# Kernel optimization log

Measured on AMD Instinct MI355X. Metric: run time of the kernel, lower is better.

## Reference

```python
import jax, jax.numpy as jnp
from jax import lax
import numpy as np

V, D_EMB, H, P, B, T = 32000, 512, 1024, 512, 32, 512
NUM_LAYERS = 2


def setup_inputs() -> dict:
    key = jax.random.key(0)
    ks = jax.random.split(key, 2 + NUM_LAYERS * 5)
    tokens = jax.random.randint(ks[0], (B, T), 0, V, dtype=jnp.int32)
    embed = jax.random.normal(ks[1], (V, D_EMB), dtype=jnp.float32) * 0.02
    inp = {"tokens": tokens, "embed": embed}
    in_dims = [D_EMB] + [P] * (NUM_LAYERS - 1)
    for l in range(NUM_LAYERS):
        kk = ks[2 + 5 * l: 7 + 5 * l]
        inp[f"Wx{l}"] = jax.random.normal(kk[0], (in_dims[l], 4 * H), dtype=jnp.float32) * 0.02
        inp[f"Wh{l}"] = jax.random.normal(kk[1], (H, 4 * H), dtype=jnp.float32) * 0.02
        inp[f"b{l}"] = jnp.zeros((4 * H,), dtype=jnp.float32)
        inp[f"Wfc{l}"] = jax.random.normal(kk[3], (H, P), dtype=jnp.float32) * 0.02
        inp[f"bfc{l}"] = jnp.zeros((P,), dtype=jnp.float32)
    return inp


def _lstm(x, Wx, Wh, b):
    # x: [B, T, D] -> [B, T, H]. Keras gate order: i, f, g(cell), o.
    Bsz = x.shape[0]
    h0 = jnp.zeros((Bsz, H), dtype=x.dtype)
    c0 = jnp.zeros((Bsz, H), dtype=x.dtype)

    # Precompute input projection for all timesteps (one big GEMM).
    xz = jnp.einsum('btd,dg->btg', x, Wx) + b  # [B, T, 4H]

    def step(carry, zt):
        h, c = carry
        z = zt + h @ Wh
        i, f, g, o = jnp.split(z, 4, axis=-1)
        c = jax.nn.sigmoid(f) * c + jax.nn.sigmoid(i) * jnp.tanh(g)
        h = jax.nn.sigmoid(o) * jnp.tanh(c)
        return (h, c), h

    _, ys = lax.scan(step, (h0, c0), jnp.swapaxes(xz, 0, 1))  # ys: [T, B, H]
    return jnp.swapaxes(ys, 0, 1)


def reference(tokens, embed, Wx0, Wh0, b0, Wfc0, bfc0, Wx1, Wh1, b1, Wfc1, bfc1):
    # inference path: dropout is identity (training=False), use_softmax=False
    x = embed[tokens]  # [B, T, D_EMB]
    layers = [(Wx0, Wh0, b0, Wfc0, bfc0), (Wx1, Wh1, b1, Wfc1, bfc1)]
    for Wx, Wh, b, Wfc, bfc in layers:
        x = _lstm(x, Wx, Wh, b)
        x = x @ Wfc + bfc  # per-layer dense projection [B, T, P]
    return x
```

## Files before the change

kernel.cpp:

```cpp
#include <hip/hip_runtime.h>
#include <cstdio>
#include <cstdint>

typedef unsigned short u16;
typedef unsigned int u32;
typedef float f32x4 __attribute__((ext_vector_type(4)));
typedef short s16x8 __attribute__((ext_vector_type(8)));

#define DI __device__ __forceinline__

#define BATCH 32
#define SEQT 512
#define HDIM 1024
#define PDIM 512
#define DEMB 512
#define G4H 4096
#define NWGR 256

DI u16 f2bf(float f) {
  u32 u = __float_as_uint(f);
  return (u16)((u + 0x7fffu + ((u >> 16) & 1u)) >> 16);
}
DI float bf2f(u16 h) { return __uint_as_float(((u32)h) << 16); }
DI void split2(float f, u16 &hi, u16 &lo) {
  hi = f2bf(f);
  lo = f2bf(f - bf2f(hi));
}
DI f32x4 mfma16(s16x8 a, s16x8 b, f32x4 c) {
  return __builtin_amdgcn_mfma_f32_16x16x32_bf16(a, b, c, 0, 0, 0);
}
DI void dma16(const void *g, void *l) {
  __builtin_amdgcn_global_load_lds((const __attribute__((address_space(1))) void *)g,
                                   (__attribute__((address_space(3))) void *)l, 16, 0, 0);
}
DI s16x8 ld128_dev(const u16 *p) {
  s16x8 r;
  asm volatile("global_load_dwordx4 %0, %1, off sc1" : "=v"(r) : "v"(p));
  return r;
}
DI void st16_dev(u16 *p, u16 v) {
  asm volatile("global_store_short %0, %1, off sc1" ::"v"(p), "v"((u32)v) : "memory");
}
DI void st32_dev(int *p, int v) {
  asm volatile("global_store_dword %0, %1, off sc1" ::"v"(p), "v"(v) : "memory");
}

__global__ void k_gather_pack(const int *__restrict__ tokens, const float *__restrict__ embed,
                              u16 *__restrict__ xhi, u16 *__restrict__ xlo) {
  int idx = blockIdx.x * 256 + threadIdx.x;
  int m = idx >> 6;
  int k8 = (idx & 63) << 3;
  int tok = tokens[m];
  const float *src = embed + (size_t)tok * DEMB + k8;
  float4 a = *(const float4 *)src;
  float4 b = *(const float4 *)(src + 4);
  float v[8] = {a.x, a.y, a.z, a.w, b.x, b.y, b.z, b.w};
  union UV { u16 h[8]; int4 v; };
  UV uh, ul;
#pragma unroll
  for (int j = 0; j < 8; ++j) split2(v[j], uh.h[j], ul.h[j]);
  size_t o = (size_t)m * DEMB + k8;
  *(int4 *)(xhi + o) = uh.v;
  *(int4 *)(xlo + o) = ul.v;
}

__global__ void k_packT(const float *__restrict__ W, u16 *__restrict__ Thi, u16 *__restrict__ Tlo,
                        int K, int N) {
  __shared__ float tile[32][33];
  int n0 = blockIdx.x * 32, k0 = blockIdx.y * 32;
  int tx = threadIdx.x, ty = threadIdx.y;
#pragma unroll
  for (int i = 0; i < 4; ++i) tile[ty + 8 * i][tx] = W[(size_t)(k0 + ty + 8 * i) * N + n0 + tx];
  __syncthreads();
#pragma unroll
  for (int i = 0; i < 4; ++i) {
    int n = ty + 8 * i;
    u16 hi, lo;
    split2(tile[tx][n], hi, lo);
    size_t o = (size_t)(n0 + n) * K + k0 + tx;
    Thi[o] = hi;
    Tlo[o] = lo;
  }
}

template <int OM>
__global__ __launch_bounds__(256, 2) void k_gemm(const u16 *__restrict__ Ahi, const u16 *__restrict__ Alo,
                                                 const u16 *__restrict__ Bhi, const u16 *__restrict__ Blo,
                                                 const float *__restrict__ bias, void *__restrict__ out0,
                                                 void *__restrict__ out1, int M, int N, int K) {
  __shared__ u16 sP[4][128 * 64];
  const int tid = threadIdx.x;
  const int w = tid >> 6, lane = tid & 63;
  const int la15 = lane & 15, la4 = lane >> 4;
  const int nbn = N >> 7;
  const int bm = blockIdx.x / nbn, bn = blockIdx.x % nbn;
  const u16 *src = (w == 0) ? Ahi : (w == 1) ? Alo : (w == 2) ? Bhi : Blo;
  const int rowbase = (w < 2) ? bm * 128 : bn * 128;
  char *lds = (char *)&sP[w][0];

  f32x4 acc[2][8] = {};
  for (int kb = 0; kb < K; kb += 64) {
#pragma unroll
    for (int i = 0; i < 16; ++i) {
      int s = i * 64 + lane;
      int row = s >> 3;
      int k16 = (s & 7) ^ (row & 7);
      dma16(src + (size_t)(rowbase + row) * K + kb + k16 * 8, lds + i * 1024);
    }
    asm volatile("s_waitcnt vmcnt(0)" ::: "memory");
    __syncthreads();
#pragma unroll
    for (int ksl = 0; ksl < 2; ++ksl) {
      s16x8 ah[2], al[2];
#pragma unroll
      for (int rf = 0; rf < 2; ++rf) {
        int row = 32 * w + 16 * rf + la15;
        int slot = row * 8 + ((4 * ksl + la4) ^ (row & 7));
        ah[rf] = *(const s16x8 *)((const char *)&sP[0][0] + slot * 16);
        al[rf] = *(const s16x8 *)((const char *)&sP[1][0] + slot * 16);
      }
#pragma unroll
      for (int cf = 0; cf < 8; ++cf) {
        int col = 16 * cf + la15;
        int slot = col * 8 + ((4 * ksl + la4) ^ (col & 7));
        s16x8 bh = *(const s16x8 *)((const char *)&sP[2][0] + slot * 16);
        s16x8 bl = *(const s16x8 *)((const char *)&sP[3][0] + slot * 16);
#pragma unroll
        for (int rf = 0; rf < 2; ++rf) {
          acc[rf][cf] = mfma16(ah[rf], bh, acc[rf][cf]);
          acc[rf][cf] = mfma16(ah[rf], bl, acc[rf][cf]);
          acc[rf][cf] = mfma16(al[rf], bh, acc[rf][cf]);
        }
      }
    }
    __syncthreads();
  }
#pragma unroll
  for (int rf = 0; rf < 2; ++rf) {
#pragma unroll
    for (int cf = 0; cf < 8; ++cf) {
      int c = bn * 128 + 16 * cf + la15;
      float bv = bias ? bias[c] : 0.f;
#pragma unroll
      for (int q = 0; q < 4; ++q) {
        int r = bm * 128 + 32 * w + 16 * rf + 4 * la4 + q;
        float v = acc[rf][cf][q] + bv;
        if (OM == 0) {
          ((u16 *)out0)[(size_t)r * N + c] = f2bf(v);
        } else if (OM == 1) {
          u16 hi, lo;
          split2(v, hi, lo);
          ((u16 *)out0)[(size_t)r * N + c] = hi;
          ((u16 *)out1)[(size_t)r * N + c] = lo;
        } else {
          int b2 = r & 31, tt = r >> 5;
          ((float *)out0)[((size_t)b2 * SEQT + tt) * PDIM + c] = v;
        }
      }
    }
  }
}

__global__ __launch_bounds__(256, 1) void k_recur(const u16 *__restrict__ xz, const float *__restrict__ Wh,
                                                  u16 *hhi, u16 *hlo, int *done, int rowmode) {
  __shared__ u16 sW[2][32 * 1024];
  __shared__ float zacc[4][16][33];
  __shared__ float sC[128];
  const int tid = threadIdx.x;
  const int w = tid >> 6, lane = tid & 63;
  const int la15 = lane & 15, la4 = lane >> 4;
  const int wg = blockIdx.x;
  const int rg = wg & 1;
  const int g = wg >> 1;

  for (int idx = tid; idx < 32 * 1024; idx += 256) {
    int zc = idx & 31;
    int k = idx >> 5;
    int gate = zc >> 3, cl = zc & 7;
    int gcol = gate * HDIM + 8 * g + cl;
    u16 hi, lo;
    split2(Wh[(size_t)k * G4H + gcol], hi, lo);
    int boff = zc * 2048 + ((((k >> 3) ^ (zc & 7))) << 4) + (k & 7) * 2;
    *(u16 *)((char *)&sW[0][0] + boff) = hi;
    *(u16 *)((char *)&sW[1][0] + boff) = lo;
  }
  if (tid < 128) sC[tid] = 0.f;
  __syncthreads();

  const int r_g = tid >> 3, hc = tid & 7;
  const int bg = 16 * rg + r_g;
  const int ks0 = 8 * w;
  const int bA = 16 * rg + la15;

  for (int t = 0; t < SEQT; ++t) {
    float xzv[4] = {0.f, 0.f, 0.f, 0.f};
    if (tid < 128) {
      size_t m = (rowmode == 0) ? ((size_t)bg * SEQT + t) : ((size_t)t * 32 + bg);
      const u16 *px = xz + m * G4H + 8 * g + hc;
#pragma unroll
      for (int gi = 0; gi < 4; ++gi) xzv[gi] = bf2f(px[(size_t)gi * HDIM]);
    }
    if (t > 0 && w == 0) {
      const int *dp = done + (size_t)(t - 1) * 256 + rg * 128 + lane;
      for (long tries = 0;; ++tries) {
        int a = __hip_atomic_load(dp, __ATOMIC_RELAXED, __HIP_MEMORY_SCOPE_AGENT);
        int b = __hip_atomic_load(dp + 64, __ATOMIC_RELAXED, __HIP_MEMORY_SCOPE_AGENT);
        if (__all((a & b) == 1)) break;
        if (tries > (1L << 22)) break;
        __builtin_amdgcn_s_sleep(1);
      }
    }
    __syncthreads();
    if (t > 0) {
      const u16 *ph = hhi + ((size_t)(t - 1) * 32 + bA) * HDIM;
      const u16 *pl = hlo + ((size_t)(t - 1) * 32 + bA) * HDIM;
      s16x8 ahi[8], alo[8];
#pragma unroll
      for (int j8 = 0; j8 < 8; ++j8) {
        int k = 32 * (ks0 + j8) + 8 * la4;
        ahi[j8] = ld128_dev(ph + k);
        alo[j8] = ld128_dev(pl + k);
      }
      asm volatile("s_waitcnt vmcnt(0)" ::: "memory");
      __builtin_amdgcn_sched_barrier(0);
      f32x4 acc[2] = {};
#pragma unroll
      for (int j8 = 0; j8 < 8; ++j8) {
#pragma unroll
        for (int cf = 0; cf < 2; ++cf) {
          int zc = 16 * cf + la15;
          int slot = (4 * (ks0 + j8) + la4) ^ (zc & 7);
          int boff = zc * 2048 + (slot << 4);
          s16x8 bh = *(const s16x8 *)((const char *)&sW[0][0] + boff);
          s16x8 bl = *(const s16x8 *)((const char *)&sW[1][0] + boff);
          acc[cf] = mfma16(ahi[j8], bh, acc[cf]);
          acc[cf] = mfma16(ahi[j8], bl, acc[cf]);
          acc[cf] = mfma16(alo[j8], bh, acc[cf]);
        }
      }
#pragma unroll
      for (int cf = 0; cf < 2; ++cf)
#pragma unroll
        for (int q = 0; q < 4; ++q) zacc[w][4 * la4 + q][16 * cf + la15] = acc[cf][q];
    }
    __syncthreads();
    if (tid < 128) {
      float z4[4];
#pragma unroll
      for (int gi = 0; gi < 4; ++gi) {
        float s = xzv[gi];
        if (t > 0) {
          int zc = gi * 8 + hc;
          s += zacc[0][r_g][zc] + zacc[1][r_g][zc] + zacc[2][r_g][zc] + zacc[3][r_g][zc];
        }
        z4[gi] = s;
      }
      float ig = 1.f / (1.f + expf(-z4[0]));
      float fg = 1.f / (1.f + expf(-z4[1]));
      float gg = tanhf(z4[2]);
      float og = 1.f / (1.f + expf(-z4[3]));
      float c = fg * sC[tid] + ig * gg;
      sC[tid] = c;
      float h = og * tanhf(c);
      u16 hi, lo;
      split2(h, hi, lo);
      size_t ho = ((size_t)t * 32 + bg) * HDIM + 8 * g + hc;
      st16_dev(hhi + ho, hi);
      st16_dev(hlo + ho, lo);
    }
    asm volatile("s_waitcnt vmcnt(0)" ::: "memory");
    __syncthreads();
    if (tid == 0) st32_dev(done + (size_t)t * 256 + rg * 128 + g, 1);
  }
}

extern "C" void kernel_launch(void *const *d_in, const int *in_sizes, int n_in,
                              void *d_out, int out_size, void *d_ws, size_t ws_size,
                              hipStream_t stream) {
  const int *tokens = (const int *)d_in[0];
  const float *embed = (const float *)d_in[1];
  const float *Wx0 = (const float *)d_in[2];
  const float *Wh0 = (const float *)d_in[3];
  const float *b0 = (const float *)d_in[4];
  const float *Wfc0 = (const float *)d_in[5];
  const float *bfc0 = (const float *)d_in[6];
  const float *Wx1 = (const float *)d_in[7];
  const float *Wh1 = (const float *)d_in[8];
  const float *b1 = (const float *)d_in[9];
  const float *Wfc1 = (const float *)d_in[10];
  const float *bfc1 = (const float *)d_in[11];

  constexpr size_t NEED = 255856640;
  if (ws_size < NEED) {
    fprintf(stderr, "RNNLM kernel: ws too small (%zu < %zu)\n", ws_size, NEED);
    return;
  }
  char *ws = (char *)d_ws;
  u16 *xz = (u16 *)(ws + 0);
  u16 *hhi = (u16 *)(ws + 134217728);
  u16 *hlo = (u16 *)(ws + 167772160);
  u16 *x1hi = (u16 *)(ws + 201326592);
  u16 *x1lo = (u16 *)(ws + 218103808);
  u16 *WxT0hi = (u16 *)(ws + 234881024);
  u16 *WxT0lo = (u16 *)(ws + 239075328);
  u16 *WfcT0hi = (u16 *)(ws + 243269632);
  u16 *WfcT0lo = (u16 *)(ws + 244318208);
  u16 *WxT1hi = (u16 *)(ws + 245366784);
  u16 *WxT1lo = (u16 *)(ws + 249561088);
  u16 *WfcT1hi = (u16 *)(ws + 253755392);
  u16 *WfcT1lo = (u16 *)(ws + 254803968);
  int *done0 = (int *)(ws + 234881024);
  int *done1 = (int *)(ws + 245366784);

  k_packT<<<dim3(G4H / 32, DEMB / 32), dim3(32, 8), 0, stream>>>(Wx0, WxT0hi, WxT0lo, DEMB, G4H);
  k_packT<<<dim3(PDIM / 32, HDIM / 32), dim3(32, 8), 0, stream>>>(Wfc0, WfcT0hi, WfcT0lo, HDIM, PDIM);
  k_packT<<<dim3(G4H / 32, DEMB / 32), dim3(32, 8), 0, stream>>>(Wx1, WxT1hi, WxT1lo, DEMB, G4H);
  k_packT<<<dim3(PDIM / 32, HDIM / 32), dim3(32, 8), 0, stream>>>(Wfc1, WfcT1hi, WfcT1lo, HDIM, PDIM);
  k_gather_pack<<<4096, 256, 0, stream>>>(tokens, embed, x1hi, x1lo);

  k_gemm<0><<<dim3(128 * 32), 256, 0, stream>>>(x1hi, x1lo, WxT0hi, WxT0lo, b0, xz, nullptr,
                                                16384, G4H, DEMB);
  hipMemsetAsync(done0, 0, SEQT * 256 * sizeof(int), stream);
  {
    const u16 *a0 = xz; const float *a1 = Wh0; u16 *a2 = hhi; u16 *a3 = hlo; int *a4 = done0; int a5 = 0;
    void *args[] = {&a0, &a1, &a2, &a3, &a4, &a5};
    hipError_t e = hipLaunchCooperativeKernel((void *)k_recur, dim3(NWGR), dim3(256), args, 0, stream);
    if (e != hipSuccess) fprintf(stderr, "coop launch L0 failed: %d\n", (int)e);
  }
  k_gemm<1><<<dim3(128 * 4), 256, 0, stream>>>(hhi, hlo, WfcT0hi, WfcT0lo, bfc0, x1hi, x1lo,
                                               16384, PDIM, HDIM);
  k_gemm<0><<<dim3(128 * 32), 256, 0, stream>>>(x1hi, x1lo, WxT1hi, WxT1lo, b1, xz, nullptr,
                                                16384, G4H, DEMB);
  hipMemsetAsync(done1, 0, SEQT * 256 * sizeof(int), stream);
  {
    const u16 *a0 = xz; const float *a1 = Wh1; u16 *a2 = hhi; u16 *a3 = hlo; int *a4 = done1; int a5 = 1;
    void *args[] = {&a0, &a1, &a2, &a3, &a4, &a5};
    hipError_t e = hipLaunchCooperativeKernel((void *)k_recur, dim3(NWGR), dim3(256), args, 0, stream);
    if (e != hipSuccess) fprintf(stderr, "coop launch L1 failed: %d\n", (int)e);
  }
  k_gemm<2><<<dim3(128 * 4), 256, 0, stream>>>(hhi, hlo, WfcT1hi, WfcT1lo, bfc1, d_out, nullptr,
                                               16384, PDIM, HDIM);
}
```

Before: 5.586 ms.

## Exchange recurrent hidden state through a double-buffered ring with monotonic step flags

The recurrent kernel now publishes each step's hidden state to a small two-slot ring buffer and reads the previous step from it, instead of from the full per-timestep history array. The full history is still written with plain stores for the following projection GEMM. The per-step done array is replaced by one monotonic counter per workgroup, so each wait polls the same addresses and the memset shrinks. The aim is to keep the hidden-state exchange and flag polling in a small, cache-resident footprint and cut latency on the serial critical path, at the cost of an extra store per element.

```diff
diff --git a/kernel.cpp b/kernel.cpp
--- a/kernel.cpp
+++ b/kernel.cpp
@@ -162,7 +162,8 @@
 }
 
 __global__ __launch_bounds__(256, 1) void k_recur(const u16 *__restrict__ xz, const float *__restrict__ Wh,
-                                                  u16 *hhi, u16 *hlo, int *done, int rowmode) {
+                                                  u16 *hist_hi, u16 *hist_lo, u16 *ring_hi, u16 *ring_lo,
+                                                  int *flags, int rowmode) {
   __shared__ u16 sW[2][32 * 1024];
   __shared__ float zacc[4][16][33];
   __shared__ float sC[128];
@@ -201,19 +202,19 @@
       for (int gi = 0; gi < 4; ++gi) xzv[gi] = bf2f(px[(size_t)gi * HDIM]);
     }
     if (t > 0 && w == 0) {
-      const int *dp = done + (size_t)(t - 1) * 256 + rg * 128 + lane;
+      const int *dp = flags + rg * 128 + lane;
       for (long tries = 0;; ++tries) {
         int a = __hip_atomic_load(dp, __ATOMIC_RELAXED, __HIP_MEMORY_SCOPE_AGENT);
         int b = __hip_atomic_load(dp + 64, __ATOMIC_RELAXED, __HIP_MEMORY_SCOPE_AGENT);
-        if (__all((a & b) == 1)) break;
+        if (__all(a >= t && b >= t)) break;
         if (tries > (1L << 22)) break;
         __builtin_amdgcn_s_sleep(1);
       }
     }
     __syncthreads();
     if (t > 0) {
-      const u16 *ph = hhi + ((size_t)(t - 1) * 32 + bA) * HDIM;
-      const u16 *pl = hlo + ((size_t)(t - 1) * 32 + bA) * HDIM;
+      const u16 *ph = ring_hi + (((size_t)((t - 1) & 1)) * 32 + bA) * HDIM;
+      const u16 *pl = ring_lo + (((size_t)((t - 1) & 1)) * 32 + bA) * HDIM;
       s16x8 ahi[8], alo[8];
 #pragma unroll
       for (int j8 = 0; j8 < 8; ++j8) {
@@ -264,13 +265,16 @@
       float h = og * tanhf(c);
       u16 hi, lo;
       split2(h, hi, lo);
+      size_t ro = (((size_t)(t & 1)) * 32 + bg) * HDIM + 8 * g + hc;
+      st16_dev(ring_hi + ro, hi);
+      st16_dev(ring_lo + ro, lo);
       size_t ho = ((size_t)t * 32 + bg) * HDIM + 8 * g + hc;
-      st16_dev(hhi + ho, hi);
-      st16_dev(hlo + ho, lo);
+      hist_hi[ho] = hi;
+      hist_lo[ho] = lo;
     }
     asm volatile("s_waitcnt vmcnt(0)" ::: "memory");
     __syncthreads();
-    if (tid == 0) st32_dev(done + (size_t)t * 256 + rg * 128 + g, 1);
+    if (tid == 0) st32_dev(flags + rg * 128 + g, t + 1);
   }
 }
 
@@ -309,8 +313,12 @@
   u16 *WxT1lo = (u16 *)(ws + 249561088);
   u16 *WfcT1hi = (u16 *)(ws + 253755392);
   u16 *WfcT1lo = (u16 *)(ws + 254803968);
-  int *done0 = (int *)(ws + 234881024);
-  int *done1 = (int *)(ws + 245366784);
+  u16 *ring0hi = (u16 *)(ws + 234881024);
+  u16 *ring0lo = (u16 *)(ws + 234881024 + 131072);
+  int *flags0 = (int *)(ws + 234881024 + 262144);
+  u16 *ring1hi = (u16 *)(ws + 245366784);
+  u16 *ring1lo = (u16 *)(ws + 245366784 + 131072);
+  int *flags1 = (int *)(ws + 245366784 + 262144);
 
   k_packT<<<dim3(G4H / 32, DEMB / 32), dim3(32, 8), 0, stream>>>(Wx0, WxT0hi, WxT0lo, DEMB, G4H);
   k_packT<<<dim3(PDIM / 32, HDIM / 32), dim3(32, 8), 0, stream>>>(Wfc0, WfcT0hi, WfcT0lo, HDIM, PDIM);
@@ -320,10 +328,11 @@
 
   k_gemm<0><<<dim3(128 * 32), 256, 0, stream>>>(x1hi, x1lo, WxT0hi, WxT0lo, b0, xz, nullptr,
                                                 16384, G4H, DEMB);
-  hipMemsetAsync(done0, 0, SEQT * 256 * sizeof(int), stream);
+  hipMemsetAsync(flags0, 0, NWGR * sizeof(int), stream);
   {
-    const u16 *a0 = xz; const float *a1 = Wh0; u16 *a2 = hhi; u16 *a3 = hlo; int *a4 = done0; int a5 = 0;
-    void *args[] = {&a0, &a1, &a2, &a3, &a4, &a5};
+    const u16 *a0 = xz; const float *a1 = Wh0; u16 *a2 = hhi; u16 *a3 = hlo;
+    u16 *a4 = ring0hi; u16 *a5 = ring0lo; int *a6 = flags0; int a7 = 0;
+    void *args[] = {&a0, &a1, &a2, &a3, &a4, &a5, &a6, &a7};
     hipError_t e = hipLaunchCooperativeKernel((void *)k_recur, dim3(NWGR), dim3(256), args, 0, stream);
     if (e != hipSuccess) fprintf(stderr, "coop launch L0 failed: %d\n", (int)e);
   }
@@ -331,10 +340,11 @@
                                                16384, PDIM, HDIM);
   k_gemm<0><<<dim3(128 * 32), 256, 0, stream>>>(x1hi, x1lo, WxT1hi, WxT1lo, b1, xz, nullptr,
                                                 16384, G4H, DEMB);
-  hipMemsetAsync(done1, 0, SEQT * 256 * sizeof(int), stream);
+  hipMemsetAsync(flags1, 0, NWGR * sizeof(int), stream);
   {
-    const u16 *a0 = xz; const float *a1 = Wh1; u16 *a2 = hhi; u16 *a3 = hlo; int *a4 = done1; int a5 = 1;
-    void *args[] = {&a0, &a1, &a2, &a3, &a4, &a5};
+    const u16 *a0 = xz; const float *a1 = Wh1; u16 *a2 = hhi; u16 *a3 = hlo;
+    u16 *a4 = ring1hi; u16 *a5 = ring1lo; int *a6 = flags1; int a7 = 1;
+    void *args[] = {&a0, &a1, &a2, &a3, &a4, &a5, &a6, &a7};
     hipError_t e = hipLaunchCooperativeKernel((void *)k_recur, dim3(NWGR), dim3(256), args, 0, stream);
     if (e != hipSuccess) fprintf(stderr, "coop launch L1 failed: %d\n", (int)e);
   }
```

Measured after the change: 5.720 ms. 2.4% more time.

## Streamline recurrent step sync with counter flags, coalesced h stores, fast gates

Applied to the files above, without the earlier changes.

The per-timestep done array is replaced by one monotonic counter per workgroup, so the flag is polled against t. The h output is staged in shared memory and written as 128-bit stores by one wave, which alone waits for them before publishing the flag. That wave is the only one storing h, so this removes the block-wide waitcnt and barrier. Workgroups are remapped so each XCD owns a contiguous column range. The h loads drop the sc1 inline asm for plain loads, and the sigmoid/tanh gates use exp2/rcp intrinsics. The goal is lower per-step latency in the serial recurrence, at the cost of slightly lower gate precision and reliance on plain loads seeing fresh cross-XCD data.

```diff
diff --git a/kernel.cpp b/kernel.cpp
--- a/kernel.cpp
+++ b/kernel.cpp
@@ -6,6 +6,7 @@
 typedef unsigned int u32;
 typedef float f32x4 __attribute__((ext_vector_type(4)));
 typedef short s16x8 __attribute__((ext_vector_type(8)));
+typedef int i32x4 __attribute__((ext_vector_type(4)));
 
 #define DI __device__ __forceinline__
 
@@ -33,17 +34,24 @@
   __builtin_amdgcn_global_load_lds((const __attribute__((address_space(1))) void *)g,
                                    (__attribute__((address_space(3))) void *)l, 16, 0, 0);
 }
-DI s16x8 ld128_dev(const u16 *p) {
-  s16x8 r;
-  asm volatile("global_load_dwordx4 %0, %1, off sc1" : "=v"(r) : "v"(p));
-  return r;
-}
-DI void st16_dev(u16 *p, u16 v) {
-  asm volatile("global_store_short %0, %1, off sc1" ::"v"(p), "v"((u32)v) : "memory");
+DI void st128_dev(u16 *p, i32x4 v) {
+  asm volatile("global_store_dwordx4 %0, %1, off sc1" ::"v"(p), "v"(v) : "memory");
 }
 DI void st32_dev(int *p, int v) {
   asm volatile("global_store_dword %0, %1, off sc1" ::"v"(p), "v"(v) : "memory");
 }
+
+#if __has_builtin(__builtin_amdgcn_exp2f) && __has_builtin(__builtin_amdgcn_rcpf)
+DI float fsig(float x) {
+  return __builtin_amdgcn_rcpf(1.f + __builtin_amdgcn_exp2f(-1.4426950408889634f * x));
+}
+DI float ftanh(float x) {
+  return 2.f * __builtin_amdgcn_rcpf(1.f + __builtin_amdgcn_exp2f(-2.8853900817779268f * x)) - 1.f;
+}
+#else
+DI float fsig(float x) { return 1.f / (1.f + expf(-x)); }
+DI float ftanh(float x) { return tanhf(x); }
+#endif
 
 __global__ void k_gather_pack(const int *__restrict__ tokens, const float *__restrict__ embed,
                               u16 *__restrict__ xhi, u16 *__restrict__ xlo) {
@@ -162,20 +170,22 @@
 }
 
 __global__ __launch_bounds__(256, 1) void k_recur(const u16 *__restrict__ xz, const float *__restrict__ Wh,
-                                                  u16 *hhi, u16 *hlo, int *done, int rowmode) {
+                                                  u16 *hist_hi, u16 *hist_lo, int *flags, int rowmode) {
   __shared__ u16 sW[2][32 * 1024];
   __shared__ float zacc[4][16][33];
   __shared__ float sC[128];
+  __shared__ __align__(16) u16 sH[2][16][8];
   const int tid = threadIdx.x;
   const int w = tid >> 6, lane = tid & 63;
   const int la15 = lane & 15, la4 = lane >> 4;
   const int wg = blockIdx.x;
-  const int rg = wg & 1;
-  const int g = wg >> 1;
-
-  for (int idx = tid; idx < 32 * 1024; idx += 256) {
-    int zc = idx & 31;
-    int k = idx >> 5;
+  const int xcd = wg & 7, idx = wg >> 3;
+  const int rg = xcd & 1;
+  const int g = (xcd >> 1) * 32 + idx;
+
+  for (int i2 = tid; i2 < 32 * 1024; i2 += 256) {
+    int zc = i2 & 31;
+    int k = i2 >> 5;
     int gate = zc >> 3, cl = zc & 7;
     int gcol = gate * HDIM + 8 * g + cl;
     u16 hi, lo;
@@ -201,28 +211,26 @@
       for (int gi = 0; gi < 4; ++gi) xzv[gi] = bf2f(px[(size_t)gi * HDIM]);
     }
     if (t > 0 && w == 0) {
-      const int *dp = done + (size_t)(t - 1) * 256 + rg * 128 + lane;
+      const int *dp = flags + rg * 128 + lane;
       for (long tries = 0;; ++tries) {
         int a = __hip_atomic_load(dp, __ATOMIC_RELAXED, __HIP_MEMORY_SCOPE_AGENT);
         int b = __hip_atomic_load(dp + 64, __ATOMIC_RELAXED, __HIP_MEMORY_SCOPE_AGENT);
-        if (__all((a & b) == 1)) break;
+        if (__all(a >= t && b >= t)) break;
         if (tries > (1L << 22)) break;
         __builtin_amdgcn_s_sleep(1);
       }
     }
     __syncthreads();
     if (t > 0) {
-      const u16 *ph = hhi + ((size_t)(t - 1) * 32 + bA) * HDIM;
-      const u16 *pl = hlo + ((size_t)(t - 1) * 32 + bA) * HDIM;
+      const u16 *ph = hist_hi + ((size_t)(t - 1) * 32 + bA) * HDIM;
+      const u16 *pl = hist_lo + ((size_t)(t - 1) * 32 + bA) * HDIM;
       s16x8 ahi[8], alo[8];
 #pragma unroll
       for (int j8 = 0; j8 < 8; ++j8) {
         int k = 32 * (ks0 + j8) + 8 * la4;
-        ahi[j8] = ld128_dev(ph + k);
-        alo[j8] = ld128_dev(pl + k);
-      }
-      asm volatile("s_waitcnt vmcnt(0)" ::: "memory");
-      __builtin_amdgcn_sched_barrier(0);
+        ahi[j8] = *(const s16x8 *)(ph + k);
+        alo[j8] = *(const s16x8 *)(pl + k);
+      }
       f32x4 acc[2] = {};
 #pragma unroll
       for (int j8 = 0; j8 < 8; ++j8) {
@@ -255,22 +263,29 @@
         }
         z4[gi] = s;
       }
-      float ig = 1.f / (1.f + expf(-z4[0]));
-      float fg = 1.f / (1.f + expf(-z4[1]));
-      float gg = tanhf(z4[2]);
-      float og = 1.f / (1.f + expf(-z4[3]));
+      float ig = fsig(z4[0]);
+      float fg = fsig(z4[1]);
+      float gg = ftanh(z4[2]);
+      float og = fsig(z4[3]);
       float c = fg * sC[tid] + ig * gg;
       sC[tid] = c;
-      float h = og * tanhf(c);
+      float h = og * ftanh(c);
       u16 hi, lo;
       split2(h, hi, lo);
-      size_t ho = ((size_t)t * 32 + bg) * HDIM + 8 * g + hc;
-      st16_dev(hhi + ho, hi);
-      st16_dev(hlo + ho, lo);
-    }
-    asm volatile("s_waitcnt vmcnt(0)" ::: "memory");
-    __syncthreads();
-    if (tid == 0) st32_dev(done + (size_t)t * 256 + rg * 128 + g, 1);
+      sH[0][r_g][hc] = hi;
+      sH[1][r_g][hc] = lo;
+    }
+    __syncthreads();
+    if (tid < 32) {
+      int p = tid >> 4, r = tid & 15;
+      i32x4 v = *(const i32x4 *)&sH[p][r][0];
+      u16 *base = p ? hist_lo : hist_hi;
+      st128_dev(base + ((size_t)t * 32 + 16 * rg + r) * HDIM + 8 * g, v);
+    }
+    if (w == 0) {
+      asm volatile("s_waitcnt vmcnt(0)" ::: "memory");
+      if (tid == 0) st32_dev(flags + rg * 128 + g, t + 1);
+    }
   }
 }
 
@@ -309,8 +324,8 @@
   u16 *WxT1lo = (u16 *)(ws + 249561088);
   u16 *WfcT1hi = (u16 *)(ws + 253755392);
   u16 *WfcT1lo = (u16 *)(ws + 254803968);
-  int *done0 = (int *)(ws + 234881024);
-  int *done1 = (int *)(ws + 245366784);
+  int *flags0 = (int *)(ws + 234881024);
+  int *flags1 = (int *)(ws + 245366784);
 
   k_packT<<<dim3(G4H / 32, DEMB / 32), dim3(32, 8), 0, stream>>>(Wx0, WxT0hi, WxT0lo, DEMB, G4H);
   k_packT<<<dim3(PDIM / 32, HDIM / 32), dim3(32, 8), 0, stream>>>(Wfc0, WfcT0hi, WfcT0lo, HDIM, PDIM);
@@ -320,9 +335,10 @@
 
   k_gemm<0><<<dim3(128 * 32), 256, 0, stream>>>(x1hi, x1lo, WxT0hi, WxT0lo, b0, xz, nullptr,
                                                 16384, G4H, DEMB);
-  hipMemsetAsync(done0, 0, SEQT * 256 * sizeof(int), stream);
+  (void)hipMemsetAsync(flags0, 0, NWGR * sizeof(int), stream);
   {
-    const u16 *a0 = xz; const float *a1 = Wh0; u16 *a2 = hhi; u16 *a3 = hlo; int *a4 = done0; int a5 = 0;
+    const u16 *a0 = xz; const float *a1 = Wh0; u16 *a2 = hhi; u16 *a3 = hlo;
+    int *a4 = flags0; int a5 = 0;
     void *args[] = {&a0, &a1, &a2, &a3, &a4, &a5};
     hipError_t e = hipLaunchCooperativeKernel((void *)k_recur, dim3(NWGR), dim3(256), args, 0, stream);
     if (e != hipSuccess) fprintf(stderr, "coop launch L0 failed: %d\n", (int)e);
@@ -331,9 +347,10 @@
                                                16384, PDIM, HDIM);
   k_gemm<0><<<dim3(128 * 32), 256, 0, stream>>>(x1hi, x1lo, WxT1hi, WxT1lo, b1, xz, nullptr,
                                                 16384, G4H, DEMB);
-  hipMemsetAsync(done1, 0, SEQT * 256 * sizeof(int), stream);
+  (void)hipMemsetAsync(flags1, 0, NWGR * sizeof(int), stream);
   {
-    const u16 *a0 = xz; const float *a1 = Wh1; u16 *a2 = hhi; u16 *a3 = hlo; int *a4 = done1; int a5 = 1;
+    const u16 *a0 = xz; const float *a1 = Wh1; u16 *a2 = hhi; u16 *a3 = hlo;
+    int *a4 = flags1; int a5 = 1;
     void *args[] = {&a0, &a1, &a2, &a3, &a4, &a5};
     hipError_t e = hipLaunchCooperativeKernel((void *)k_recur, dim3(NWGR), dim3(256), args, 0, stream);
     if (e != hipSuccess) fprintf(stderr, "coop launch L1 failed: %d\n", (int)e);
```

After: 6.545 ms. 1.17x slower.
